# Performance work log

Measured on AMD Instinct MI355X. Metric: run time of the kernel, lower is better.

The kernel has to match this reference:

```python
import jax, jax.numpy as jnp
import numpy as np
import math

NUM_HEADS = 16


def setup_inputs() -> dict:
    key = jax.random.key(0)
    ks = jax.random.split(key, 5)
    B, C, H = 2, 2048, 1024
    return {
        "x": jax.random.normal(ks[0], (B, C, H), dtype=jnp.float32),
        "Wqkv_w": jax.random.normal(ks[1], (3 * H, H), dtype=jnp.float32) * (1.0 / math.sqrt(H)),
        "Wqkv_b": jax.random.normal(ks[2], (3 * H,), dtype=jnp.float32) * 0.02,
        "Wo_w": jax.random.normal(ks[3], (H, H), dtype=jnp.float32) * (1.0 / math.sqrt(H)),
        "Wo_b": jax.random.normal(ks[4], (H,), dtype=jnp.float32) * 0.02,
    }


def reference(x, Wqkv_w, Wqkv_b, Wo_w, Wo_b):
    B, C, H = x.shape
    nh = NUM_HEADS
    hd = H // nh
    # QKV projection (torch Linear: x @ W.T + b)
    qkv = x @ Wqkv_w.T + Wqkv_b                      # [B, C, 3H]
    qkv = qkv.reshape(B, C, 3, nh, hd)
    qkv = jnp.transpose(qkv, (2, 0, 3, 1, 4))        # [3, B, nh, C, hd]
    q, k, v = qkv[0], qkv[1], qkv[2]
    scale = 1.0 / math.sqrt(hd)
    att = jnp.einsum('bhqd,bhkd->bhqk', q, k) * scale  # [B, nh, C, C]
    causal = jnp.triu(jnp.ones((C, C), dtype=bool), k=1)  # True above diagonal
    att = jnp.where(causal[None, None], jnp.float32(-jnp.inf), att)
    att = jax.nn.softmax(att, axis=-1)
    # dropout p set to 0 (eval-mode math)
    out = jnp.einsum('bhqk,bhkd->bhqd', att, v)       # [B, nh, C, hd]
    out = jnp.transpose(out, (0, 2, 1, 3)).reshape(B, C, H)
    return out @ Wo_w.T + Wo_b
```

## Files before the change

### kernel.cpp

```cpp
#include <hip/hip_runtime.h>
#include <hip/hip_bf16.h>
#include <math.h>

typedef unsigned short u16;
typedef __attribute__((ext_vector_type(8))) __bf16 bf16x8;
typedef __attribute__((ext_vector_type(4))) float f32x4;
typedef __attribute__((ext_vector_type(8))) unsigned short u16x8;
typedef __attribute__((ext_vector_type(4))) unsigned int u32x4;

__device__ __forceinline__ u16 f2bf(float f) {
  union { float f; unsigned u; } x; x.f = f;
  unsigned r = x.u + 0x7fffu + ((x.u >> 16) & 1u);
  return (u16)(r >> 16);
}

__device__ __forceinline__ void gload16(const u16* g, u16* l) {
  __builtin_amdgcn_global_load_lds(
      (const __attribute__((address_space(1))) void*)g,
      (__attribute__((address_space(3))) void*)l, 16, 0, 0);
}

#define MFMA16(a, b, c) __builtin_amdgcn_mfma_f32_16x16x32_bf16((a), (b), (c), 0, 0, 0)

__global__ __launch_bounds__(256) void cast_bf16_kernel(
    const float* __restrict__ in, u16* __restrict__ out, int n4) {
  int i = blockIdx.x * 256 + threadIdx.x;
  if (i >= n4) return;
  f32x4 v = *(const f32x4*)(in + (size_t)i * 4);
  u16 o0 = f2bf(v[0]), o1 = f2bf(v[1]), o2 = f2bf(v[2]), o3 = f2bf(v[3]);
  unsigned lo = (unsigned)o0 | ((unsigned)o1 << 16);
  unsigned hi = (unsigned)o2 | ((unsigned)o3 << 16);
  ((unsigned*)out)[(size_t)i * 2] = lo;
  ((unsigned*)out)[(size_t)i * 2 + 1] = hi;
}

__device__ __forceinline__ void gemm_bt_128(
    const u16* __restrict__ A, const u16* __restrict__ B, int K, int m0, int n0,
    u16* As, u16* Bs, f32x4 acc[4][4]) {
  const int tid = threadIdx.x;
  const int lane = tid & 63;
  const int wr = tid >> 7;
  const int wc = (tid >> 6) & 1;
  for (int k0 = 0; k0 < K; k0 += 64) {
    #pragma unroll
    for (int it = 0; it < 4; ++it) {
      int c = it * 256 + tid;
      int row = c >> 3;
      int ko = (c & 7) << 3;
      gload16(A + (size_t)(m0 + row) * K + (k0 + ko), As + c * 8);
      gload16(B + (size_t)(n0 + row) * K + (k0 + ko), Bs + c * 8);
    }
    __syncthreads();
    #pragma unroll
    for (int kk = 0; kk < 2; ++kk) {
      bf16x8 a[4], b[4];
      #pragma unroll
      for (int m = 0; m < 4; ++m)
        a[m] = *(const bf16x8*)(As + ((wr * 64 + m * 16 + (lane & 15)) * 64 +
                                      kk * 32 + ((lane >> 4) << 3)));
      #pragma unroll
      for (int n = 0; n < 4; ++n)
        b[n] = *(const bf16x8*)(Bs + ((wc * 64 + n * 16 + (lane & 15)) * 64 +
                                      kk * 32 + ((lane >> 4) << 3)));
      #pragma unroll
      for (int m = 0; m < 4; ++m)
        #pragma unroll
        for (int n = 0; n < 4; ++n)
          acc[m][n] = MFMA16(a[m], b[n], acc[m][n]);
    }
    __syncthreads();
  }
}

__global__ __launch_bounds__(256) void gemm_qkv_kernel(
    const u16* __restrict__ X, const u16* __restrict__ W, const float* __restrict__ bias,
    u16* __restrict__ Qb, u16* __restrict__ Kb, u16* __restrict__ Vb) {
  __shared__ __align__(16) u16 As[128 * 64];
  __shared__ __align__(16) u16 Bs[128 * 64];
  f32x4 acc[4][4];
  #pragma unroll
  for (int m = 0; m < 4; ++m)
    #pragma unroll
    for (int n = 0; n < 4; ++n) acc[m][n] = (f32x4){0.f, 0.f, 0.f, 0.f};
  const int m0 = blockIdx.y * 128;
  const int n0 = blockIdx.x * 128;
  gemm_bt_128(X, W, 1024, m0, n0, As, Bs, acc);
  const int lane = threadIdx.x & 63;
  const int wr = threadIdx.x >> 7, wc = (threadIdx.x >> 6) & 1;
  #pragma unroll
  for (int m = 0; m < 4; ++m) {
    #pragma unroll
    for (int n = 0; n < 4; ++n) {
      #pragma unroll
      for (int j = 0; j < 4; ++j) {
        int row = m0 + wr * 64 + m * 16 + ((lane >> 4) << 2) + j;
        int col = n0 + wc * 64 + n * 16 + (lane & 15);
        float v = acc[m][n][j] + bias[col];
        int which = col >> 10;
        int rem = col & 1023;
        int h = rem >> 6, d = rem & 63;
        int bb = row >> 11, q = row & 2047;
        if (which == 0) v *= 0.125f;
        u16* dst = (which == 0) ? Qb : (which == 1 ? Kb : Vb);
        dst[((size_t)((bb * 16 + h) * 2048 + q)) * 64 + d] = f2bf(v);
      }
    }
  }
}

__global__ __launch_bounds__(256) void gemm_out_kernel(
    const u16* __restrict__ Ain, const u16* __restrict__ W, const float* __restrict__ bias,
    float* __restrict__ out) {
  __shared__ __align__(16) u16 As[128 * 64];
  __shared__ __align__(16) u16 Bs[128 * 64];
  f32x4 acc[4][4];
  #pragma unroll
  for (int m = 0; m < 4; ++m)
    #pragma unroll
    for (int n = 0; n < 4; ++n) acc[m][n] = (f32x4){0.f, 0.f, 0.f, 0.f};
  const int m0 = blockIdx.y * 128;
  const int n0 = blockIdx.x * 128;
  gemm_bt_128(Ain, W, 1024, m0, n0, As, Bs, acc);
  const int lane = threadIdx.x & 63;
  const int wr = threadIdx.x >> 7, wc = (threadIdx.x >> 6) & 1;
  #pragma unroll
  for (int m = 0; m < 4; ++m) {
    #pragma unroll
    for (int n = 0; n < 4; ++n) {
      #pragma unroll
      for (int j = 0; j < 4; ++j) {
        int row = m0 + wr * 64 + m * 16 + ((lane >> 4) << 2) + j;
        int col = n0 + wc * 64 + n * 16 + (lane & 15);
        out[(size_t)row * 1024 + col] = acc[m][n][j] + bias[col];
      }
    }
  }
}

__device__ __forceinline__ void attn_one(
    const u16* __restrict__ Qh, const u16* __restrict__ Kh, const u16* __restrict__ Vh,
    u16* __restrict__ Ob, int bb, int h, int qt,
    u16 (*Ks)[64 * 64], u16 (*Vt)[64 * 64]) {
  const int tid = threadIdx.x, lane = tid & 63, w = tid >> 6;
  const int g = lane >> 4, q15 = lane & 15;

  bf16x8 qf[2];
  const int qrow = qt * 64 + w * 16 + q15;
  #pragma unroll
  for (int kk = 0; kk < 2; ++kk)
    qf[kk] = *(const bf16x8*)(Qh + (size_t)qrow * 64 + kk * 32 + g * 8);

  f32x4 acc_o[4];
  #pragma unroll
  for (int n = 0; n < 4; ++n) acc_o[n] = (f32x4){0.f, 0.f, 0.f, 0.f};
  float m_run = -INFINITY, l_run = 0.f;

  const int nt = qt + 1;

  auto stageK = [&](int t, int buf) {
    #pragma unroll
    for (int it = 0; it < 2; ++it) {
      int c = it * 256 + tid;
      int row = c >> 3, b8 = c & 7;
      gload16(Kh + (size_t)(t * 64 + row) * 64 + ((b8 ^ (row & 7)) << 3),
              Ks[buf] + c * 8);
    }
  };

  stageK(0, 0);
  #pragma unroll
  for (int it = 0; it < 2; ++it) {
    int kloc = it * 32 + (tid >> 3);
    int d0 = (tid & 7) << 3;
    u16x8 v = *(const u16x8*)(Vh + (size_t)kloc * 64 + d0);
    #pragma unroll
    for (int i = 0; i < 8; ++i) {
      int d = d0 + i;
      int fv = (d + (d >> 3)) & 7;
      Vt[0][d * 64 + (((kloc >> 3) ^ fv) << 3) + (kloc & 7)] = v[i];
    }
  }
  __syncthreads();

  for (int t = 0; t < nt; ++t) {
    const int cur = t & 1;
    const bool pre = (t + 1 < nt);
    u16x8 vreg[2];
    if (pre) {
      stageK(t + 1, cur ^ 1);
      #pragma unroll
      for (int it = 0; it < 2; ++it) {
        int kloc = it * 32 + (tid >> 3);
        int d0 = (tid & 7) << 3;
        vreg[it] = *(const u16x8*)(Vh + (size_t)((t + 1) * 64 + kloc) * 64 + d0);
      }
    }

    f32x4 accs[4];
    __builtin_amdgcn_s_setprio(1);
    #pragma unroll
    for (int cb = 0; cb < 4; ++cb) {
      accs[cb] = (f32x4){0.f, 0.f, 0.f, 0.f};
      #pragma unroll
      for (int kk = 0; kk < 2; ++kk) {
        int row = cb * 16 + q15;
        int kblk = kk * 4 + g;
        bf16x8 kf = *(const bf16x8*)(Ks[cur] + row * 64 + ((kblk ^ (row & 7)) << 3));
        accs[cb] = MFMA16(kf, qf[kk], accs[cb]);
      }
    }
    __builtin_amdgcn_s_setprio(0);
    if (t == nt - 1) {
      #pragma unroll
      for (int cb = 0; cb < 4; ++cb)
        #pragma unroll
        for (int j = 0; j < 4; ++j) {
          int kg = t * 64 + cb * 16 + 4 * g + j;
          int qg = qt * 64 + w * 16 + q15;
          if (kg > qg) accs[cb][j] = -INFINITY;
        }
    }

    float mj = accs[0][0];
    #pragma unroll
    for (int cb = 0; cb < 4; ++cb)
      #pragma unroll
      for (int j = 0; j < 4; ++j) mj = fmaxf(mj, accs[cb][j]);
    mj = fmaxf(mj, __shfl_xor(mj, 16));
    mj = fmaxf(mj, __shfl_xor(mj, 32));
    float mn = fmaxf(m_run, mj);
    float sc = __expf(m_run - mn);
    m_run = mn;
    float rs = 0.f;
    #pragma unroll
    for (int cb = 0; cb < 4; ++cb)
      #pragma unroll
      for (int j = 0; j < 4; ++j) {
        float p = __expf(accs[cb][j] - mn);
        accs[cb][j] = p;
        rs += p;
      }
    rs += __shfl_xor(rs, 16);
    rs += __shfl_xor(rs, 32);
    l_run = l_run * sc + rs;

    float scj[4];
    #pragma unroll
    for (int j = 0; j < 4; ++j) scj[j] = __shfl(sc, 4 * g + j);
    #pragma unroll
    for (int n = 0; n < 4; ++n)
      #pragma unroll
      for (int j = 0; j < 4; ++j) acc_o[n][j] *= scj[j];

    unsigned Wp[4][2];
    #pragma unroll
    for (int cb = 0; cb < 4; ++cb)
      #pragma unroll
      for (int hh = 0; hh < 2; ++hh)
        asm("v_cvt_pk_bf16_f32 %0, %1, %2"
            : "=v"(Wp[cb][hh]) : "v"(accs[cb][2 * hh]), "v"(accs[cb][2 * hh + 1]));

    unsigned aw[2][4];
    #pragma unroll
    for (int kk = 0; kk < 2; ++kk)
      #pragma unroll
      for (int iw = 0; iw < 4; ++iw) {
        int srcLane = q15 + ((((g & 1) << 1) + (iw >> 1)) << 4);
        unsigned c0 = __shfl(Wp[2 * kk + 0][iw & 1], srcLane);
        unsigned c1 = __shfl(Wp[2 * kk + 1][iw & 1], srcLane);
        aw[kk][iw] = (g >> 1) ? c1 : c0;
      }
    bf16x8 pa0 = __builtin_bit_cast(bf16x8, (u32x4){aw[0][0], aw[0][1], aw[0][2], aw[0][3]});
    bf16x8 pa1 = __builtin_bit_cast(bf16x8, (u32x4){aw[1][0], aw[1][1], aw[1][2], aw[1][3]});

    __builtin_amdgcn_s_setprio(1);
    #pragma unroll
    for (int n = 0; n < 4; ++n) {
      #pragma unroll
      for (int kk = 0; kk < 2; ++kk) {
        int cblk = kk * 4 + g;
        int d = n * 16 + q15;
        int fv = (d + (d >> 3)) & 7;
        bf16x8 vb = *(const bf16x8*)(Vt[cur] + d * 64 + ((cblk ^ fv) << 3));
        acc_o[n] = MFMA16(kk ? pa1 : pa0, vb, acc_o[n]);
      }
    }
    __builtin_amdgcn_s_setprio(0);

    if (pre) {
      #pragma unroll
      for (int it = 0; it < 2; ++it) {
        int kloc = it * 32 + (tid >> 3);
        int d0 = (tid & 7) << 3;
        #pragma unroll
        for (int i = 0; i < 8; ++i) {
          int d = d0 + i;
          int fv = (d + (d >> 3)) & 7;
          Vt[cur ^ 1][d * 64 + (((kloc >> 3) ^ fv) << 3) + (kloc & 7)] = vreg[it][i];
        }
      }
    }
    __syncthreads();
  }

  float invl = 1.0f / l_run;
  float invj[4];
  #pragma unroll
  for (int j = 0; j < 4; ++j) invj[j] = __shfl(invl, 4 * g + j);
  #pragma unroll
  for (int n = 0; n < 4; ++n)
    #pragma unroll
    for (int j = 0; j < 4; ++j) {
      int qg = qt * 64 + w * 16 + 4 * g + j;
      Ob[((size_t)(bb * 2048 + qg)) * 1024 + h * 64 + n * 16 + q15] =
          f2bf(acc_o[n][j] * invj[j]);
    }
}

__global__ __launch_bounds__(256, 4) void attn_kernel(
    const u16* __restrict__ Qb, const u16* __restrict__ Kb, const u16* __restrict__ Vb,
    u16* __restrict__ Ob) {
  __shared__ __align__(16) u16 Ks[2][64 * 64];
  __shared__ __align__(16) u16 Vt[2][64 * 64];
  const int blk = blockIdx.x;
  const int p = blk & 15;
  const int bh = blk >> 4;
  const size_t base = (size_t)bh * 2048 * 64;
  const int bb = bh >> 4, h = bh & 15;
  attn_one(Qb + base, Kb + base, Vb + base, Ob, bb, h, 31 - p, Ks, Vt);
  attn_one(Qb + base, Kb + base, Vb + base, Ob, bb, h, p, Ks, Vt);
}

extern "C" void kernel_launch(void* const* d_in, const int* in_sizes, int n_in,
                              void* d_out, int out_size, void* d_ws, size_t ws_size,
                              hipStream_t stream) {
  const float* x    = (const float*)d_in[0];
  const float* wqkv = (const float*)d_in[1];
  const float* bqkv = (const float*)d_in[2];
  const float* wo   = (const float*)d_in[3];
  const float* bo   = (const float*)d_in[4];
  float* out = (float*)d_out;

  const size_t MB = 1u << 20;
  char* ws = (char*)d_ws;
  u16* x_bf  = (u16*)(ws);
  u16* wq_bf = (u16*)(ws + 8 * MB);
  u16* wo_bf = (u16*)(ws + 14 * MB);
  u16* q_buf = (u16*)(ws + 16 * MB);
  u16* k_buf = (u16*)(ws + 24 * MB);
  u16* v_buf = (u16*)(ws + 32 * MB);
  u16* a_out = (u16*)(ws + 40 * MB);

  cast_bf16_kernel<<<4096, 256, 0, stream>>>(x, x_bf, 1048576);
  cast_bf16_kernel<<<3072, 256, 0, stream>>>(wqkv, wq_bf, 786432);
  cast_bf16_kernel<<<1024, 256, 0, stream>>>(wo, wo_bf, 262144);

  gemm_qkv_kernel<<<dim3(24, 32), 256, 0, stream>>>(x_bf, wq_bf, bqkv,
                                                    q_buf, k_buf, v_buf);
  attn_kernel<<<512, 256, 0, stream>>>(q_buf, k_buf, v_buf, a_out);
  gemm_out_kernel<<<dim3(8, 32), 256, 0, stream>>>(a_out, wo_bf, bo, out);
}
```

Before: 153.4 us.

## Fuse cast kernels, fold log2e into Q scale, retile output GEMM to 64x128

The three fp32-to-bf16 cast launches become one kernel that selects its source by index range, removing two launches. The Q scale now folds in log2(e), so the softmax can use exp2f in place of __expf. The output projection GEMM moves to 64x128 tiles with four waves each covering 32 columns, doubling the grid to 512 blocks so more CUs stay busy on the small M=4096,N=1024 problem. Per-block reuse drops and the new K loop has no double buffering.

```diff
diff --git a/kernel.cpp b/kernel.cpp
--- a/kernel.cpp
+++ b/kernel.cpp
@@ -22,16 +22,23 @@
 
 #define MFMA16(a, b, c) __builtin_amdgcn_mfma_f32_16x16x32_bf16((a), (b), (c), 0, 0, 0)
 
-__global__ __launch_bounds__(256) void cast_bf16_kernel(
-    const float* __restrict__ in, u16* __restrict__ out, int n4) {
+#define QSCALE 0.18033688011112043f
+
+__global__ __launch_bounds__(256) void cast_all_kernel(
+    const float* __restrict__ x, const float* __restrict__ wqkv,
+    const float* __restrict__ wo, u16* __restrict__ xb,
+    u16* __restrict__ wqb, u16* __restrict__ wob) {
   int i = blockIdx.x * 256 + threadIdx.x;
-  if (i >= n4) return;
-  f32x4 v = *(const f32x4*)(in + (size_t)i * 4);
+  const float* src; u16* dst;
+  if (i < 1048576)      { src = x;    dst = xb;  }
+  else if (i < 1835008) { src = wqkv; dst = wqb; i -= 1048576; }
+  else                  { src = wo;   dst = wob; i -= 1835008; }
+  f32x4 v = *(const f32x4*)(src + (size_t)i * 4);
   u16 o0 = f2bf(v[0]), o1 = f2bf(v[1]), o2 = f2bf(v[2]), o3 = f2bf(v[3]);
   unsigned lo = (unsigned)o0 | ((unsigned)o1 << 16);
   unsigned hi = (unsigned)o2 | ((unsigned)o3 << 16);
-  ((unsigned*)out)[(size_t)i * 2] = lo;
-  ((unsigned*)out)[(size_t)i * 2 + 1] = hi;
+  ((unsigned*)dst)[(size_t)i * 2] = lo;
+  ((unsigned*)dst)[(size_t)i * 2 + 1] = hi;
 }
 
 __device__ __forceinline__ void gemm_bt_128(
@@ -100,7 +107,7 @@
         int rem = col & 1023;
         int h = rem >> 6, d = rem & 63;
         int bb = row >> 11, q = row & 2047;
-        if (which == 0) v *= 0.125f;
+        if (which == 0) v *= QSCALE;
         u16* dst = (which == 0) ? Qb : (which == 1 ? Kb : Vb);
         dst[((size_t)((bb * 16 + h) * 2048 + q)) * 64 + d] = f2bf(v);
       }
@@ -111,30 +118,55 @@
 __global__ __launch_bounds__(256) void gemm_out_kernel(
     const u16* __restrict__ Ain, const u16* __restrict__ W, const float* __restrict__ bias,
     float* __restrict__ out) {
-  __shared__ __align__(16) u16 As[128 * 64];
+  __shared__ __align__(16) u16 As[64 * 64];
   __shared__ __align__(16) u16 Bs[128 * 64];
-  f32x4 acc[4][4];
+  const int tid = threadIdx.x;
+  const int lane = tid & 63;
+  const int wc = tid >> 6;
+  const int m0 = blockIdx.y * 64;
+  const int n0 = blockIdx.x * 128;
+  f32x4 acc[4][2] = {};
+  for (int k0 = 0; k0 < 1024; k0 += 64) {
+    #pragma unroll
+    for (int it = 0; it < 2; ++it) {
+      int c = it * 256 + tid;
+      gload16(Ain + (size_t)(m0 + (c >> 3)) * 1024 + k0 + ((c & 7) << 3), As + c * 8);
+    }
+    #pragma unroll
+    for (int it = 0; it < 4; ++it) {
+      int c = it * 256 + tid;
+      gload16(W + (size_t)(n0 + (c >> 3)) * 1024 + k0 + ((c & 7) << 3), Bs + c * 8);
+    }
+    __syncthreads();
+    #pragma unroll
+    for (int kk = 0; kk < 2; ++kk) {
+      bf16x8 a[4], b[2];
+      #pragma unroll
+      for (int m = 0; m < 4; ++m)
+        a[m] = *(const bf16x8*)(As + ((m * 16 + (lane & 15)) * 64 +
+                                      kk * 32 + ((lane >> 4) << 3)));
+      #pragma unroll
+      for (int n = 0; n < 2; ++n)
+        b[n] = *(const bf16x8*)(Bs + ((wc * 32 + n * 16 + (lane & 15)) * 64 +
+                                      kk * 32 + ((lane >> 4) << 3)));
+      #pragma unroll
+      for (int m = 0; m < 4; ++m)
+        #pragma unroll
+        for (int n = 0; n < 2; ++n)
+          acc[m][n] = MFMA16(a[m], b[n], acc[m][n]);
+    }
+    __syncthreads();
+  }
   #pragma unroll
   for (int m = 0; m < 4; ++m)
     #pragma unroll
-    for (int n = 0; n < 4; ++n) acc[m][n] = (f32x4){0.f, 0.f, 0.f, 0.f};
-  const int m0 = blockIdx.y * 128;
-  const int n0 = blockIdx.x * 128;
-  gemm_bt_128(Ain, W, 1024, m0, n0, As, Bs, acc);
-  const int lane = threadIdx.x & 63;
-  const int wr = threadIdx.x >> 7, wc = (threadIdx.x >> 6) & 1;
-  #pragma unroll
-  for (int m = 0; m < 4; ++m) {
-    #pragma unroll
-    for (int n = 0; n < 4; ++n) {
+    for (int n = 0; n < 2; ++n)
       #pragma unroll
       for (int j = 0; j < 4; ++j) {
-        int row = m0 + wr * 64 + m * 16 + ((lane >> 4) << 2) + j;
-        int col = n0 + wc * 64 + n * 16 + (lane & 15);
+        int row = m0 + m * 16 + ((lane >> 4) << 2) + j;
+        int col = n0 + wc * 32 + n * 16 + (lane & 15);
         out[(size_t)row * 1024 + col] = acc[m][n][j] + bias[col];
       }
-    }
-  }
 }
 
 __device__ __forceinline__ void attn_one(
@@ -216,8 +248,7 @@
         #pragma unroll
         for (int j = 0; j < 4; ++j) {
           int kg = t * 64 + cb * 16 + 4 * g + j;
-          int qg = qt * 64 + w * 16 + q15;
-          if (kg > qg) accs[cb][j] = -INFINITY;
+          if (kg > qrow) accs[cb][j] = -INFINITY;
         }
     }
 
@@ -229,14 +260,14 @@
     mj = fmaxf(mj, __shfl_xor(mj, 16));
     mj = fmaxf(mj, __shfl_xor(mj, 32));
     float mn = fmaxf(m_run, mj);
-    float sc = __expf(m_run - mn);
+    float sc = exp2f(m_run - mn);
     m_run = mn;
     float rs = 0.f;
     #pragma unroll
     for (int cb = 0; cb < 4; ++cb)
       #pragma unroll
       for (int j = 0; j < 4; ++j) {
-        float p = __expf(accs[cb][j] - mn);
+        float p = exp2f(accs[cb][j] - mn);
         accs[cb][j] = p;
         rs += p;
       }
@@ -351,12 +382,10 @@
   u16* v_buf = (u16*)(ws + 32 * MB);
   u16* a_out = (u16*)(ws + 40 * MB);
 
-  cast_bf16_kernel<<<4096, 256, 0, stream>>>(x, x_bf, 1048576);
-  cast_bf16_kernel<<<3072, 256, 0, stream>>>(wqkv, wq_bf, 786432);
-  cast_bf16_kernel<<<1024, 256, 0, stream>>>(wo, wo_bf, 262144);
+  cast_all_kernel<<<8192, 256, 0, stream>>>(x, wqkv, wo, x_bf, wq_bf, wo_bf);
 
   gemm_qkv_kernel<<<dim3(24, 32), 256, 0, stream>>>(x_bf, wq_bf, bqkv,
                                                     q_buf, k_buf, v_buf);
   attn_kernel<<<512, 256, 0, stream>>>(q_buf, k_buf, v_buf, a_out);
-  gemm_out_kernel<<<dim3(8, 32), 256, 0, stream>>>(a_out, wo_bf, bo, out);
-}
+  gemm_out_kernel<<<dim3(8, 64), 256, 0, stream>>>(a_out, wo_bf, bo, out);
+}
```

Result: no change. 151.4 us (-1.3%).
